# Kernel optimization log

Hardware: AMD Instinct MI355X
Metric: run time of the kernel (lower is better)

## Reference

```python
import jax, jax.numpy as jnp
import numpy as np
from jax import lax


def conv1x1(x, w, b=None):
    # x: [B,C,H,W], w: [O,C]
    y = jnp.einsum('bchw,oc->bohw', x, w)
    if b is not None:
        y = y + b[None, :, None, None]
    return y


def conv1x9(x, w, b):
    # x: [B,C,H,W], w: [O,I,1,9], pad (0,4) -> same spatial size
    y = lax.conv_general_dilated(x, w, window_strides=(1, 1),
                                 padding=((0, 0), (4, 4)),
                                 dimension_numbers=('NCHW', 'OIHW', 'NCHW'))
    return y + b[None, :, None, None]


def skn(inputs, fc1_w, fc2_w):
    # Selective Kernel fusion: M=len(inputs), each [B,C,H,W]
    M = len(inputs)
    B, C = inputs[0].shape[0], inputs[0].shape[1]
    U = inputs[0]
    for t in inputs[1:]:
        U = U + t
    s = U.mean(axis=(2, 3))                               # [B,C] global avg pool
    z = jax.nn.leaky_relu(jnp.einsum('bc,oc->bo', s, fc1_w), 0.01)
    ab = jnp.einsum('bo,po->bp', z, fc2_w).reshape(B, M, C)
    a = jax.nn.softmax(ab, axis=1)                        # softmax over branches
    out = inputs[0] * a[:, 0][:, :, None, None]
    for i in range(1, M):
        out = out + inputs[i] * a[:, i][:, :, None, None]
    return out


def setup_inputs() -> dict:
    key = jax.random.key(0)
    ks = jax.random.split(key, 24)
    B, C, H, W = 2, 128, 128, 512
    Ch = C // 2
    p = lambda k, shp: (jax.random.normal(k, shp, jnp.float32) * 0.02)
    d = {}
    d['left_feat'] = jax.random.normal(ks[0], (B, C, H, W), jnp.float32)
    d['right_feat'] = jax.random.normal(ks[1], (B, C, H, W), jnp.float32)
    d['emb_l_w'] = p(ks[2], (Ch, C)); d['emb_l_b'] = p(ks[3], (Ch,))
    d['emb_r_w'] = p(ks[4], (Ch, C)); d['emb_r_b'] = p(ks[5], (Ch,))
    d['emb_lv_w'] = p(ks[6], (Ch, C)); d['emb_lv_b'] = p(ks[7], (Ch,))
    d['emb_rv_w'] = p(ks[8], (Ch, C)); d['emb_rv_b'] = p(ks[9], (Ch,))
    d['out_l_w'] = p(ks[10], (C, Ch)); d['out_l_b'] = p(ks[11], (C,))
    d['head_w'] = p(ks[12], (C, 2 * C)); d['head_b'] = p(ks[13], (C,))
    d['body_w1'] = p(ks[14], (3, C, C, 1, 9)); d['body_b1'] = p(ks[15], (3, C))
    d['body_w2'] = p(ks[16], (3, C, C, 1, 9)); d['body_b2'] = p(ks[17], (3, C))
    d['skn1_fc1_w'] = p(ks[18], (C // 4, C)); d['skn1_fc2_w'] = p(ks[19], (3 * C, C // 4))
    d['skn2_fc1_w'] = p(ks[20], (C // 4, C)); d['skn2_fc2_w'] = p(ks[21], (3 * C, C // 4))
    d['num_window'] = 4
    return d


def reference(left_feat, right_feat, emb_l_w, emb_l_b, emb_r_w, emb_r_b,
              emb_lv_w, emb_lv_b, emb_rv_w, emb_rv_b, out_l_w, out_l_b,
              head_w, head_b, body_w1, body_b1, body_w2, body_b2,
              skn1_fc1_w, skn1_fc2_w, skn2_fc1_w, skn2_fc2_w, num_window):
    B, C, H, W = left_feat.shape
    Ch = C // 2
    nw = int(num_window)
    win = W // nw

    Q = conv1x1(left_feat, emb_l_w, emb_l_b)     # [B,Ch,H,W]
    K = conv1x1(right_feat, emb_r_w, emb_r_b)
    V_left = conv1x1(left_feat, emb_lv_w, emb_lv_b)   # computed but unused (source bug)
    V_right = conv1x1(right_feat, emb_rv_w, emb_rv_b)

    # windowed per-row cross attention over width
    Qw = Q.transpose(0, 2, 3, 1).reshape(B, H, nw, win, Ch)   # [B,H,n,q,c]
    Kw = K.transpose(0, 2, 3, 1).reshape(B, H, nw, win, Ch)   # [B,H,n,k,c]
    Vr = V_right.transpose(0, 2, 3, 1).reshape(B, H, nw, win, Ch)

    score = jnp.einsum('bhnqc,bhnkc->bhnqk', Qw, Kw)          # [B,H,n,q,k]
    M_r2l = jax.nn.softmax(score, axis=-1)
    out = jnp.einsum('bhnqk,bhnkc->bhnqc', M_r2l, Vr)         # [B,H,n,q,c]
    warped = out.reshape(B, H, W, Ch).transpose(0, 3, 1, 2)   # [B,Ch,H,W]
    left_feat_warped = jax.nn.relu(conv1x1(warped, out_l_w, out_l_b))
    # NOTE: source code (num_window>1 branch) reuses M_right_to_left and V_right
    # for the right warp as well -> right_feat_warped == left_feat_warped.
    right_feat_warped = left_feat_warped

    # head conv + 3 residual blocks (1x9 convs)
    mixed = jax.nn.relu(conv1x1(jnp.concatenate([left_feat, right_feat], axis=1),
                                head_w, head_b))
    x = mixed
    for i in range(3):
        r = jax.nn.relu(conv1x9(x, body_w1[i], body_b1[i]))
        r = conv1x9(r, body_w2[i], body_b2[i])
        x = x + r
    mixed_feat = x

    left_out = skn([left_feat, left_feat_warped, mixed_feat], skn1_fc1_w, skn1_fc2_w)
    right_out = skn([right_feat, right_feat_warped, mixed_feat], skn2_fc1_w, skn2_fc2_w)
    return (left_out, right_out)
```

## Files before the change

### kernel.cpp

```cpp
#include <hip/hip_runtime.h>
#include <hip/hip_bf16.h>

typedef __attribute__((ext_vector_type(8))) short bf16x8;
typedef __attribute__((ext_vector_type(4))) float f32x4;
typedef unsigned short u16;
typedef unsigned int u32;

#define DI __device__ __forceinline__
#define MFMA16(a, b, c) __builtin_amdgcn_mfma_f32_16x16x32_bf16((a), (b), (c), 0, 0, 0)

constexpr int Hh = 128, Ww = 512;
constexpr int HW = 65536;
constexpr long FULL = 16777216;
constexpr long HALF = 8388608;

__device__ __align__(16) u16 g_buf[2 * FULL];
__device__ __align__(16) u16 g_w[950272];
__device__ __align__(16) float g_bias[1216];
__device__ __align__(16) float g_fc[32768];
__device__ __align__(16) float g_pools[1024];
__device__ __align__(16) float g_gates[1536];
__device__ __align__(16) float g_ppart[524288];
__device__ int g_flag;

constexpr int EMB_L = 0, EMB_R = 8192, EMB_RV = 16384, HEAD = 24576, OUTL = 57344, BODY = 65536;
constexpr int B_EMBL = 0, B_EMBR = 64, B_EMBRV = 128, B_OUTL = 192, B_HEAD = 320, B_B1 = 448, B_B2 = 832;
constexpr int FC1A = 0, FC2A = 4096, FC1B = 16384, FC2B = 20480;

DI float b2f(u16 u) { union { u32 i; float f; } v; v.i = (u32)u << 16; return v.f; }
DI u16 f2b(float f) {
  union { float fl; u32 u; } v; v.fl = f;
  return (u16)((v.u + 0x7FFFu + ((v.u >> 16) & 1u)) >> 16);
}
DI float ldf(const void* p, long i, int f) {
  return f ? ((const float*)p)[i] : b2f(((const u16*)p)[i]);
}
DI bf16x8 ld8(const void* p) { return *reinterpret_cast<const bf16x8*>(p); }
DI void gload16(const u16* src, char* lds_dst) {
  __builtin_amdgcn_global_load_lds(
      (const __attribute__((address_space(1))) void*)src,
      (__attribute__((address_space(3))) void*)lds_dst, 16, 0, 0);
}

__global__ void k_detect(const void* left) {
  if (threadIdx.x != 0 || blockIdx.x != 0) return;
  const u16* pu = (const u16*)left;
  int okb = 0;
  for (int i = 0; i < 256; i++) {
    float x = b2f(pu[i]);
    float a = fabsf(x);
    if (x == 0.f || (a > 1e-8f && a < 1e4f)) okb++;
  }
  g_flag = (okb >= 230) ? 0 : 1;
}

__global__ void k_pack(const void* w1, const void* w2, const void* embl, const void* embr,
                       const void* embrv, const void* outl, const void* head,
                       const void* embl_b, const void* embr_b, const void* embrv_b,
                       const void* outl_b, const void* head_b, const void* b1, const void* b2,
                       const void* f1a, const void* f2a, const void* f1b, const void* f2b_) {
  int f = g_flag;
  int i = blockIdx.x * 256 + threadIdx.x;
  int job = blockIdx.y;
  if (job == 0) {
    if (i >= 884736) return;
    int c = i & 127, o = (i >> 7) & 127;
    int rest = i >> 14;
    int t = rest % 9, bc = rest / 9;
    const void* src = (bc & 1) ? w2 : w1;
    int blk = bc >> 1;
    g_w[BODY + i] = f2b(ldf(src, (((long)(blk * 128 + o) * 128 + c)) * 9 + t, f));
  } else if (job == 1) {
    if (i >= 65536) return;
    float v;
    if (i < 8192) v = ldf(embl, i, f);
    else if (i < 16384) v = ldf(embr, i - 8192, f);
    else if (i < 24576) v = ldf(embrv, i - 16384, f);
    else if (i < 57344) v = ldf(head, i - 24576, f);
    else v = ldf(outl, i - 57344, f);
    g_w[i] = f2b(v);
  } else if (job == 2) {
    if (i >= 1216) return;
    float v;
    if (i < 64) v = ldf(embl_b, i, f);
    else if (i < 128) v = ldf(embr_b, i - 64, f);
    else if (i < 192) v = ldf(embrv_b, i - 128, f);
    else if (i < 320) v = ldf(outl_b, i - 192, f);
    else if (i < 448) v = ldf(head_b, i - 320, f);
    else if (i < 832) v = ldf(b1, i - 448, f);
    else v = ldf(b2, i - 832, f);
    g_bias[i] = v;
  } else {
    if (i >= 32768) return;
    float v;
    if (i < 4096) v = ldf(f1a, i, f);
    else if (i < 16384) v = ldf(f2a, i - 4096, f);
    else if (i < 20480) v = ldf(f1b, i - 16384, f);
    else v = ldf(f2b_, i - 20480, f);
    g_fc[i] = v;
  }
}

__global__ __launch_bounds__(256) void k_nchw2nhwc(const void* srcL, const void* srcR,
                                                   u16* __restrict__ dstL, u16* __restrict__ dstR) {
  __shared__ u16 tile[64][130];
  int f = g_flag;
  int w0 = blockIdx.x * 64;
  int h = blockIdx.y;
  int b = blockIdx.z & 1;
  int img = blockIdx.z >> 1;
  const void* src = img ? srcR : srcL;
  u16* dst = img ? dstR : dstL;
  int t = threadIdx.x;
  int wq = (t & 31) * 2, cb = t >> 5;
  for (int c0 = 0; c0 < 128; c0 += 8) {
    int c = c0 + cb;
    long base = (long)(b * 128 + c) * HW + h * Ww + w0 + wq;
    if (f) {
      float2 v = *reinterpret_cast<const float2*>((const float*)src + base);
      tile[wq][c] = f2b(v.x);
      tile[wq + 1][c] = f2b(v.y);
    } else {
      u32 v = *reinterpret_cast<const u32*>((const u16*)src + base);
      tile[wq][c] = (u16)v;
      tile[wq + 1][c] = (u16)(v >> 16);
    }
  }
  __syncthreads();
  int c = t & 127, wb = t >> 7;
  long obase = (long)b * HW + (long)h * Ww + w0;
  for (int w1i = 0; w1i < 64; w1i += 2) {
    int w = w1i + wb;
    dst[(obase + w) * 128 + c] = tile[w][c];
  }
  if (t < 128) {
    float s = 0.f;
#pragma unroll
    for (int w = 0; w < 64; w++) s += b2f(tile[w][t]);
    g_ppart[((img * 2 + b) * 128 + t) * 1024 + (h * 8 + blockIdx.x)] = s;
  }
}

template<int K, int N, bool RELU, bool NCHW_OUT>
__global__ __launch_bounds__(256) void k_gemm1x1(const u16* __restrict__ xt, const u16* __restrict__ w,
                                                 const float* __restrict__ bias, u16* __restrict__ out,
                                                 int wstride) {
  extern __shared__ __align__(16) char smem[];
  constexpr int SLOTS = (K * 2) / 16;
  constexpr int RB = K * 2;
  int t = threadIdx.x;
  long p0 = (long)blockIdx.x * 128;
  for (int u = t; u < 128 * SLOTS; u += 256) {
    int row = u / SLOTS, slot = u % SLOTS;
    int4 v = *reinterpret_cast<const int4*>(xt + (p0 + row) * K + slot * 8);
    *reinterpret_cast<int4*>(smem + (((u32)(row * RB + slot * 16)) ^ ((row & 7) << 4))) = v;
  }
  __syncthreads();
  int wid = t >> 6, lane = t & 63, l15 = lane & 15, l4 = lane >> 4;
  constexpr int WAVES_M = (N == 64) ? 4 : 2;
  constexpr int MF = (128 / WAVES_M) / 16;
  int wm = (N == 64) ? wid : (wid >> 1);
  int wn = (N == 64) ? 0 : (wid & 1);
  int prow0 = wm * (128 / WAVES_M);
  int ocol0 = wn * 64;
  f32x4 zz = {0.f, 0.f, 0.f, 0.f};
  f32x4 acc[MF][4];
#pragma unroll
  for (int m = 0; m < MF; m++)
#pragma unroll
    for (int n = 0; n < 4; n++) acc[m][n] = zz;
#pragma unroll
  for (int k0 = 0; k0 < K; k0 += 32) {
    bf16x8 a[MF], bw[4];
#pragma unroll
    for (int m = 0; m < MF; m++) {
      int row = prow0 + m * 16 + l15;
      a[m] = ld8(smem + (((u32)(row * RB + (k0 + l4 * 8) * 2)) ^ ((row & 7) << 4)));
    }
#pragma unroll
    for (int n = 0; n < 4; n++) {
      int o = ocol0 + n * 16 + l15;
      bw[n] = ld8(w + (long)o * wstride + k0 + l4 * 8);
    }
#pragma unroll
    for (int m = 0; m < MF; m++)
#pragma unroll
      for (int n = 0; n < 4; n++) acc[m][n] = MFMA16(a[m], bw[n], acc[m][n]);
  }
  if constexpr (!NCHW_OUT) {
#pragma unroll
    for (int m = 0; m < MF; m++)
#pragma unroll
      for (int n = 0; n < 4; n++) {
        int o = ocol0 + n * 16 + l15;
        float bb = bias[o];
#pragma unroll
        for (int r = 0; r < 4; r++) {
          long p = p0 + prow0 + m * 16 + l4 * 4 + r;
          float v = acc[m][n][r] + bb;
          if (RELU) v = fmaxf(v, 0.f);
          out[p * N + o] = f2b(v);
        }
      }
  } else {
    __syncthreads();
    u16* tb = reinterpret_cast<u16*>(smem) + wid * (64 * 66);
#pragma unroll
    for (int m = 0; m < MF; m++)
#pragma unroll
      for (int n = 0; n < 4; n++) {
        float bb = bias[ocol0 + n * 16 + l15];
#pragma unroll
        for (int r = 0; r < 4; r++) {
          int pl = m * 16 + l4 * 4 + r;
          float v = acc[m][n][r] + bb;
          if (RELU) v = fmaxf(v, 0.f);
          tb[(n * 16 + l15) * 66 + pl] = f2b(v);
        }
      }
    __syncthreads();
    int bq = (int)(p0 / HW);
    int rem = (int)(p0 % HW);
    int hq = rem / Ww, wq0 = rem % Ww;
    for (int o = 0; o < 64; o++) {
      out[((long)(bq * 128 + ocol0 + o)) * HW + hq * Ww + wq0 + prow0 + lane] = tb[o * 66 + lane];
    }
  }
}

__global__ __launch_bounds__(256) void k_head(const u16* lt, const u16* rt,
                                              const u16* __restrict__ wh, const float* __restrict__ bh,
                                              u16* out) {
  extern __shared__ __align__(16) char smem[];
  int t = threadIdx.x;
  long p0 = (long)blockIdx.x * 128;
  for (int u = t; u < 2048; u += 256) {
    int row = u >> 4, slot = u & 15;
    u32 db = ((u32)(row * 256 + slot * 16)) ^ ((row & 7) << 4);
    *reinterpret_cast<int4*>(smem + db) = *reinterpret_cast<const int4*>(lt + (p0 + row) * 128 + slot * 8);
    *reinterpret_cast<int4*>(smem + 32768 + db) = *reinterpret_cast<const int4*>(rt + (p0 + row) * 128 + slot * 8);
  }
  __syncthreads();
  int wid = t >> 6, lane = t & 63, l15 = lane & 15, l4 = lane >> 4;
  int prow0 = (wid >> 1) * 64, ocol0 = (wid & 1) * 64;
  f32x4 zz = {0.f, 0.f, 0.f, 0.f};
  f32x4 acc[4][4];
#pragma unroll
  for (int m = 0; m < 4; m++)
#pragma unroll
    for (int n = 0; n < 4; n++) acc[m][n] = zz;
#pragma unroll
  for (int kk = 0; kk < 8; kk++) {
    int k0 = kk * 32;
    const char* sb = smem + ((kk >= 4) ? 32768 : 0);
    int kl = k0 & 127;
    bf16x8 a[4], bw[4];
#pragma unroll
    for (int m = 0; m < 4; m++) {
      int row = prow0 + m * 16 + l15;
      a[m] = ld8(sb + (((u32)(row * 256 + (kl + l4 * 8) * 2)) ^ ((row & 7) << 4)));
    }
#pragma unroll
    for (int n = 0; n < 4; n++) {
      int o = ocol0 + n * 16 + l15;
      bw[n] = ld8(wh + o * 256 + k0 + l4 * 8);
    }
#pragma unroll
    for (int m = 0; m < 4; m++)
#pragma unroll
      for (int n = 0; n < 4; n++) acc[m][n] = MFMA16(a[m], bw[n], acc[m][n]);
  }
  __syncthreads();
#pragma unroll
  for (int m = 0; m < 4; m++)
#pragma unroll
    for (int n = 0; n < 4; n++) {
      int o = ocol0 + n * 16 + l15;
      float bb = bh[o];
#pragma unroll
      for (int r = 0; r < 4; r++) {
        long p = p0 + prow0 + m * 16 + l4 * 4 + r;
        float v = fmaxf(acc[m][n][r] + bb, 0.f);
        out[p * 128 + o] = f2b(v);
      }
    }
}

__global__ __launch_bounds__(256) void k_attn(const u16* __restrict__ qt, const u16* __restrict__ kt,
                                              const u16* __restrict__ vt, u16* __restrict__ outT) {
  extern __shared__ __align__(16) char smem[];
  int n = blockIdx.x, h = blockIdx.y, b = blockIdx.z;
  long rb = ((long)(b * Hh + h)) * Ww + n * 128;
  int t = threadIdx.x;
  for (int u = t; u < 1024; u += 256) {
    int row = u >> 3, slot = u & 7;
    u32 db = ((u32)(row * 128 + slot * 16)) ^ ((row & 7) << 4);
    *reinterpret_cast<int4*>(smem + db) = *reinterpret_cast<const int4*>(qt + (rb + row) * 64 + slot * 8);
    *reinterpret_cast<int4*>(smem + 16384 + db) = *reinterpret_cast<const int4*>(kt + (rb + row) * 64 + slot * 8);
  }
  __syncthreads();
  int wid = t >> 6, lane = t & 63, l15 = lane & 15, l4 = lane >> 4;
  int q0 = wid * 32;
  f32x4 zz = {0.f, 0.f, 0.f, 0.f};
  f32x4 sc[2][8];
#pragma unroll
  for (int m = 0; m < 2; m++)
#pragma unroll
    for (int nf = 0; nf < 8; nf++) sc[m][nf] = zz;
#pragma unroll
  for (int k0 = 0; k0 < 64; k0 += 32) {
    bf16x8 aq[2], bk[8];
#pragma unroll
    for (int m = 0; m < 2; m++) {
      int row = q0 + m * 16 + l15;
      aq[m] = ld8(smem + (((u32)(row * 128 + (k0 + l4 * 8) * 2)) ^ ((row & 7) << 4)));
    }
#pragma unroll
    for (int nf = 0; nf < 8; nf++) {
      int row = nf * 16 + l15;
      bk[nf] = ld8(smem + 16384 + (((u32)(row * 128 + (k0 + l4 * 8) * 2)) ^ ((row & 7) << 4)));
    }
#pragma unroll
    for (int m = 0; m < 2; m++)
#pragma unroll
      for (int nf = 0; nf < 8; nf++) sc[m][nf] = MFMA16(aq[m], bk[nf], sc[m][nf]);
  }
  float rsum[2][4];
#pragma unroll
  for (int m = 0; m < 2; m++) {
#pragma unroll
    for (int r = 0; r < 4; r++) {
      float mx = -3.0e38f;
#pragma unroll
      for (int nf = 0; nf < 8; nf++) mx = fmaxf(mx, sc[m][nf][r]);
      mx = fmaxf(mx, __shfl_xor(mx, 1));
      mx = fmaxf(mx, __shfl_xor(mx, 2));
      mx = fmaxf(mx, __shfl_xor(mx, 4));
      mx = fmaxf(mx, __shfl_xor(mx, 8));
      int ql = q0 + m * 16 + l4 * 4 + r;
      float ssum = 0.f;
#pragma unroll
      for (int nf = 0; nf < 8; nf++) {
        float e = __expf(sc[m][nf][r] - mx);
        ssum += e;
        int k = nf * 16 + l15;
        *reinterpret_cast<u16*>(smem + 32768 + (((u32)(ql * 256 + k * 2)) ^ ((ql & 7) << 4))) = f2b(e);
      }
      ssum += __shfl_xor(ssum, 1);
      ssum += __shfl_xor(ssum, 2);
      ssum += __shfl_xor(ssum, 4);
      ssum += __shfl_xor(ssum, 8);
      rsum[m][r] = ssum;
    }
  }
  __syncthreads();
  for (int u = t; u < 8192; u += 256) {
    int k = u >> 6, c = u & 63;
    u16 v = vt[(rb + k) * 64 + c];
    *reinterpret_cast<u16*>(smem + (((u32)(c * 256 + k * 2)) ^ ((c & 7) << 4))) = v;
  }
  __syncthreads();
  f32x4 ov[2][4];
#pragma unroll
  for (int m = 0; m < 2; m++)
#pragma unroll
    for (int nf = 0; nf < 4; nf++) ov[m][nf] = zz;
#pragma unroll
  for (int k0 = 0; k0 < 128; k0 += 32) {
    bf16x8 ap[2], bv[4];
#pragma unroll
    for (int m = 0; m < 2; m++) {
      int row = q0 + m * 16 + l15;
      ap[m] = ld8(smem + 32768 + (((u32)(row * 256 + (k0 + l4 * 8) * 2)) ^ ((row & 7) << 4)));
    }
#pragma unroll
    for (int nf = 0; nf < 4; nf++) {
      int c = nf * 16 + l15;
      bv[nf] = ld8(smem + (((u32)(c * 256 + (k0 + l4 * 8) * 2)) ^ ((c & 7) << 4)));
    }
#pragma unroll
    for (int m = 0; m < 2; m++)
#pragma unroll
      for (int nf = 0; nf < 4; nf++) ov[m][nf] = MFMA16(ap[m], bv[nf], ov[m][nf]);
  }
#pragma unroll
  for (int m = 0; m < 2; m++)
#pragma unroll
    for (int nf = 0; nf < 4; nf++)
#pragma unroll
      for (int r = 0; r < 4; r++) {
        int q = q0 + m * 16 + l4 * 4 + r;
        int c = nf * 16 + l15;
        outT[(rb + q) * 64 + c] = f2b(ov[m][nf][r] / rsum[m][r]);
      }
}

template<bool RELU, bool HASRES, bool NCHW_OUT>
__global__ __launch_bounds__(256) void k_conv1x9(const u16* __restrict__ xin, const u16* __restrict__ wp9,
                                                 const float* __restrict__ bias, const u16* __restrict__ res,
                                                 u16* __restrict__ out) {
  __shared__ __align__(16) char xs[34816];
  __shared__ __align__(16) char wbuf[16384];
  int w0 = blockIdx.x * 128;
  int h = blockIdx.y, b = blockIdx.z;
  long rowg = ((long)(b * Hh + h)) * Ww;
  int t = threadIdx.x;
  int wid = t >> 6;
  auto stage = [&](int s) {
    int tap = s >> 2, kk = s & 3;
    const u16* base = wp9 + tap * 16384 + kk * 32;
#pragma unroll
    for (int j = 0; j < 2; j++) {
      int fidx = j * 256 + t;
      const u16* src = base + (fidx >> 2) * 128 + (fidx & 3) * 8;
      gload16(src, wbuf + (s & 1) * 8192 + j * 4096 + wid * 1024);
    }
  };
  for (int u = t; u < 2176; u += 256) {
    int row = u >> 4, slot = u & 15;
    int wg = w0 - 4 + row;
    int4 v{0, 0, 0, 0};
    if (wg >= 0 && wg < Ww) v = *reinterpret_cast<const int4*>(xin + (rowg + wg) * 128 + slot * 8);
    *reinterpret_cast<int4*>(xs + (((u32)(row * 256 + slot * 16)) ^ ((row & 7) << 4))) = v;
  }
  stage(0);
  __syncthreads();
  int lane = t & 63, l15 = lane & 15, l4 = lane >> 4;
  int p0w = (wid >> 1) * 64, o0w = (wid & 1) * 64;
  f32x4 zz = {0.f, 0.f, 0.f, 0.f};
  f32x4 acc[4][4];
#pragma unroll
  for (int m = 0; m < 4; m++)
#pragma unroll
    for (int n = 0; n < 4; n++) acc[m][n] = zz;
#pragma unroll 2
  for (int s = 0; s < 36; s++) {
    if (s < 35) stage(s + 1);
    int tap = s >> 2, kk = s & 3;
    bf16x8 a[4], bw[4];
#pragma unroll
    for (int n = 0; n < 4; n++)
      bw[n] = ld8(wbuf + (s & 1) * 8192 + (o0w + n * 16 + l15) * 64 + l4 * 16);
#pragma unroll
    for (int m = 0; m < 4; m++) {
      int row = p0w + m * 16 + l15 + tap;
      a[m] = ld8(xs + (((u32)(row * 256 + (kk * 32 + l4 * 8) * 2)) ^ ((row & 7) << 4)));
    }
#pragma unroll
    for (int m = 0; m < 4; m++)
#pragma unroll
      for (int n = 0; n < 4; n++) acc[m][n] = MFMA16(a[m], bw[n], acc[m][n]);
    __syncthreads();
  }
  float bb[4];
#pragma unroll
  for (int n = 0; n < 4; n++) bb[n] = bias[o0w + n * 16 + l15];
  if constexpr (!NCHW_OUT) {
#pragma unroll
    for (int m = 0; m < 4; m++)
#pragma unroll
      for (int n = 0; n < 4; n++) {
        int o = o0w + n * 16 + l15;
#pragma unroll
        for (int r = 0; r < 4; r++) {
          int p = w0 + p0w + m * 16 + l4 * 4 + r;
          float v = acc[m][n][r] + bb[n];
          if (RELU) v = fmaxf(v, 0.f);
          if (HASRES) v += b2f(res[(rowg + p) * 128 + o]);
          out[(rowg + p) * 128 + o] = f2b(v);
        }
      }
  } else {
    u16* tb = reinterpret_cast<u16*>(xs) + wid * (64 * 66);
#pragma unroll
    for (int m = 0; m < 4; m++)
#pragma unroll
      for (int n = 0; n < 4; n++) {
        int o = o0w + n * 16 + l15;
#pragma unroll
        for (int r = 0; r < 4; r++) {
          int pl = m * 16 + l4 * 4 + r;
          int p = w0 + p0w + pl;
          float v = acc[m][n][r] + bb[n];
          if (RELU) v = fmaxf(v, 0.f);
          if (HASRES) v += b2f(res[(rowg + p) * 128 + o]);
          tb[(n * 16 + l15) * 66 + pl] = f2b(v);
        }
      }
    __syncthreads();
    for (int o = 0; o < 64; o++) {
      out[((long)(b * 128 + o0w + o)) * HW + h * Ww + w0 + p0w + lane] = tb[o * 66 + lane];
    }
  }
}

__global__ __launch_bounds__(256) void k_pool(const u16* __restrict__ lfw, const u16* __restrict__ mixed) {
  int c = blockIdx.x, b = blockIdx.y, ts = blockIdx.z;
  float s = 0.f;
  if (ts < 2) {
    const float* pp = g_ppart + ((ts * 2 + b) * 128 + c) * 1024;
    for (int i = threadIdx.x; i < 1024; i += 256) s += pp[i];
  } else {
    long base = ((long)(b * 128 + c)) * HW;
    const u16* pu = (ts == 2) ? lfw + base : mixed + base;
    for (int i = threadIdx.x * 8; i < HW; i += 2048) {
      union { int4 v; u16 u[8]; } x;
      x.v = *reinterpret_cast<const int4*>(pu + i);
#pragma unroll
      for (int j = 0; j < 8; j++) s += b2f(x.u[j]);
    }
  }
#pragma unroll
  for (int m = 1; m < 64; m <<= 1) s += __shfl_xor(s, m);
  __shared__ float red[4];
  if ((threadIdx.x & 63) == 0) red[threadIdx.x >> 6] = s;
  __syncthreads();
  if (threadIdx.x == 0)
    g_pools[(ts * 2 + b) * 128 + c] = (red[0] + red[1] + red[2] + red[3]) * (1.f / HW);
}

__global__ void k_gate() {
  __shared__ float sv[128], zv[32];
  int b = blockIdx.x, s = blockIdx.y;
  int t = threadIdx.x;
  sv[t] = g_pools[(s * 2 + b) * 128 + t] + g_pools[(4 + b) * 128 + t] + g_pools[(6 + b) * 128 + t];
  __syncthreads();
  const float* fc1 = g_fc + (s ? FC1B : FC1A);
  const float* fc2 = g_fc + (s ? FC2B : FC2A);
  if (t < 32) {
    float z = 0.f;
    for (int c = 0; c < 128; c++) z += fc1[t * 128 + c] * sv[c];
    zv[t] = (z > 0.f) ? z : 0.01f * z;
  }
  __syncthreads();
  float ab[3];
#pragma unroll
  for (int i = 0; i < 3; i++) {
    float a = 0.f;
    for (int j = 0; j < 32; j++) a += fc2[(i * 128 + t) * 32 + j] * zv[j];
    ab[i] = a;
  }
  float mx = fmaxf(ab[0], fmaxf(ab[1], ab[2]));
  float e0 = __expf(ab[0] - mx), e1 = __expf(ab[1] - mx), e2 = __expf(ab[2] - mx);
  float inv = 1.f / (e0 + e1 + e2);
  g_gates[((s * 2 + b) * 3 + 0) * 128 + t] = e0 * inv;
  g_gates[((s * 2 + b) * 3 + 1) * 128 + t] = e1 * inv;
  g_gates[((s * 2 + b) * 3 + 2) * 128 + t] = e2 * inv;
}

__global__ __launch_bounds__(256) void k_skn_out(const void* left, const void* right,
                                                 const u16* __restrict__ lfw, const u16* __restrict__ mixed,
                                                 void* doutv) {
  int chunk = blockIdx.x, c = blockIdx.y, b = blockIdx.z;
  int f = g_flag;
  const float* g1 = g_gates + (b * 3) * 128 + c;
  const float* g2 = g_gates + ((2 + b) * 3) * 128 + c;
  float a10 = g1[0], a11 = g1[128], a12 = g1[256];
  float a20 = g2[0], a21 = g2[128], a22 = g2[256];
  long off = ((long)(b * 128 + c)) * HW + chunk * 2048 + threadIdx.x * 8;
  float xl[8], xr[8];
  if (f) {
    const float* L = (const float*)left + off;
    const float* R = (const float*)right + off;
    float4 a0 = *reinterpret_cast<const float4*>(L);
    float4 a1 = *reinterpret_cast<const float4*>(L + 4);
    float4 r0 = *reinterpret_cast<const float4*>(R);
    float4 r1 = *reinterpret_cast<const float4*>(R + 4);
    xl[0]=a0.x; xl[1]=a0.y; xl[2]=a0.z; xl[3]=a0.w; xl[4]=a1.x; xl[5]=a1.y; xl[6]=a1.z; xl[7]=a1.w;
    xr[0]=r0.x; xr[1]=r0.y; xr[2]=r0.z; xr[3]=r0.w; xr[4]=r1.x; xr[5]=r1.y; xr[6]=r1.z; xr[7]=r1.w;
  } else {
    union { int4 v; u16 u[8]; } a, r;
    a.v = *reinterpret_cast<const int4*>((const u16*)left + off);
    r.v = *reinterpret_cast<const int4*>((const u16*)right + off);
#pragma unroll
    for (int j = 0; j < 8; j++) { xl[j] = b2f(a.u[j]); xr[j] = b2f(r.u[j]); }
  }
  union { int4 v; u16 u[8]; } vw, vm;
  vw.v = *reinterpret_cast<const int4*>(lfw + off);
  vm.v = *reinterpret_cast<const int4*>(mixed + off);
  float ol[8], orr[8];
#pragma unroll
  for (int j = 0; j < 8; j++) {
    float fw = b2f(vw.u[j]), fm = b2f(vm.u[j]);
    ol[j] = a10 * xl[j] + a11 * fw + a12 * fm;
    orr[j] = a20 * xr[j] + a21 * fw + a22 * fm;
  }
  if (f) {
    float* fo = (float*)doutv;
    *reinterpret_cast<float4*>(fo + off) = make_float4(ol[0], ol[1], ol[2], ol[3]);
    *reinterpret_cast<float4*>(fo + off + 4) = make_float4(ol[4], ol[5], ol[6], ol[7]);
    *reinterpret_cast<float4*>(fo + FULL + off) = make_float4(orr[0], orr[1], orr[2], orr[3]);
    *reinterpret_cast<float4*>(fo + FULL + off + 4) = make_float4(orr[4], orr[5], orr[6], orr[7]);
  } else {
    u16* bo = (u16*)doutv;
    union { int4 v; u16 u[8]; } o1, o2;
#pragma unroll
    for (int j = 0; j < 8; j++) { o1.u[j] = f2b(ol[j]); o2.u[j] = f2b(orr[j]); }
    *reinterpret_cast<int4*>(bo + off) = o1.v;
    *reinterpret_cast<int4*>(bo + FULL + off) = o2.v;
  }
}

extern "C" void kernel_launch(void* const* d_in, const int* in_sizes, int n_in,
                              void* d_out, int out_size, void* d_ws, size_t ws_size,
                              hipStream_t stream) {
  (void)in_sizes; (void)n_in; (void)out_size; (void)d_ws; (void)ws_size;
  const void* left    = d_in[0];
  const void* right   = d_in[1];

  u16* gbuf = nullptr;
  (void)hipGetSymbolAddress((void**)&gbuf, HIP_SYMBOL(g_buf));
  u16* gw = nullptr;
  (void)hipGetSymbolAddress((void**)&gw, HIP_SYMBOL(g_w));
  float* gbias = nullptr;
  (void)hipGetSymbolAddress((void**)&gbias, HIP_SYMBOL(g_bias));

  u16* du = (u16*)d_out;
  u16* leftT   = du;
  u16* rA      = du;
  u16* rightT  = du + FULL;
  u16* xG      = du + FULL;
  u16* QT      = gbuf;
  u16* KT      = gbuf + HALF;
  u16* VrT     = gbuf + FULL;
  u16* warpedT = gbuf + FULL + HALF;
  u16* lfw     = gbuf;
  u16* mixed   = gbuf + FULL;

  k_detect<<<dim3(1), dim3(64), 0, stream>>>(left);
  k_pack<<<dim3(3456, 4), dim3(256), 0, stream>>>(
      d_in[14], d_in[16], d_in[2], d_in[4], d_in[8], d_in[10], d_in[12],
      d_in[3], d_in[5], d_in[9], d_in[11], d_in[13], d_in[15], d_in[17],
      d_in[18], d_in[19], d_in[20], d_in[21]);
  k_nchw2nhwc<<<dim3(8, 128, 4), dim3(256), 0, stream>>>(left, right, leftT, rightT);
  k_gemm1x1<128, 64, false, false><<<dim3(1024), dim3(256), 32768, stream>>>(leftT, gw + EMB_L, gbias + B_EMBL, QT, 128);
  k_gemm1x1<128, 64, false, false><<<dim3(1024), dim3(256), 32768, stream>>>(rightT, gw + EMB_R, gbias + B_EMBR, KT, 128);
  k_gemm1x1<128, 64, false, false><<<dim3(1024), dim3(256), 32768, stream>>>(rightT, gw + EMB_RV, gbias + B_EMBRV, VrT, 128);
  k_head<<<dim3(1024), dim3(256), 65536, stream>>>(leftT, rightT, gw + HEAD, gbias + B_HEAD, xG);
  k_attn<<<dim3(4, 128, 2), dim3(256), 65536, stream>>>(QT, KT, VrT, warpedT);
  k_gemm1x1<64, 128, true, true><<<dim3(1024), dim3(256), 33792, stream>>>(warpedT, gw + OUTL, gbias + B_OUTL, lfw, 64);
  for (int i = 0; i < 3; i++) {
    k_conv1x9<true, false, false><<<dim3(4, 128, 2), dim3(256), 0, stream>>>(
        xG, gw + BODY + (long)(i * 2 + 0) * 9 * 16384, gbias + B_B1 + i * 128, nullptr, rA);
    if (i < 2)
      k_conv1x9<false, true, false><<<dim3(4, 128, 2), dim3(256), 0, stream>>>(
          rA, gw + BODY + (long)(i * 2 + 1) * 9 * 16384, gbias + B_B2 + i * 128, xG, xG);
    else
      k_conv1x9<false, true, true><<<dim3(4, 128, 2), dim3(256), 0, stream>>>(
          rA, gw + BODY + (long)(i * 2 + 1) * 9 * 16384, gbias + B_B2 + i * 128, xG, mixed);
  }
  k_pool<<<dim3(128, 2, 4), dim3(256), 0, stream>>>(lfw, mixed);
  k_gate<<<dim3(2, 2), dim3(128), 0, stream>>>();
  k_skn_out<<<dim3(32, 128, 2), dim3(256), 0, stream>>>(left, right, lfw, mixed, d_out);
}
```

Baseline: 581.9 us.

## Triple-buffer conv1x9 weight staging with prefetch distance two and swizzled LDS

The 1x9 conv kernel moves from a double-buffered weight stage to a three-slot ring that prefetches two K-steps ahead. Each iteration now waits with explicit vmcnt counts and a raw s_barrier instead of a full __syncthreads, so global-to-LDS weight loads can overlap more MFMA work. Weight rows are also XOR-swizzled in LDS to reduce bank conflicts on the B-fragment reads. In exchange it uses more LDS per block, which may lower occupancy, and the correctness of the hand-written waitcnt counts depends on how gload16 is lowered.

```diff
diff --git a/kernel.cpp b/kernel.cpp
--- a/kernel.cpp
+++ b/kernel.cpp
@@ -400,20 +400,21 @@
                                                  const float* __restrict__ bias, const u16* __restrict__ res,
                                                  u16* __restrict__ out) {
   __shared__ __align__(16) char xs[34816];
-  __shared__ __align__(16) char wbuf[16384];
+  __shared__ __align__(16) char wbuf[24576];
   int w0 = blockIdx.x * 128;
   int h = blockIdx.y, b = blockIdx.z;
   long rowg = ((long)(b * Hh + h)) * Ww;
   int t = threadIdx.x;
   int wid = t >> 6;
-  auto stage = [&](int s) {
+  auto stage = [&](int s, int buf) {
     int tap = s >> 2, kk = s & 3;
     const u16* base = wp9 + tap * 16384 + kk * 32;
 #pragma unroll
     for (int j = 0; j < 2; j++) {
-      int fidx = j * 256 + t;
-      const u16* src = base + (fidx >> 2) * 128 + (fidx & 3) * 8;
-      gload16(src, wbuf + (s & 1) * 8192 + j * 4096 + wid * 1024);
+      int u = j * 256 + t;
+      int o = u >> 2, sl = u & 3;
+      int l = sl ^ (o & 3);
+      gload16(base + o * 128 + l * 8, wbuf + buf * 8192 + j * 4096 + wid * 1024);
     }
   };
   for (int u = t; u < 2176; u += 256) {
@@ -423,8 +424,11 @@
     if (wg >= 0 && wg < Ww) v = *reinterpret_cast<const int4*>(xin + (rowg + wg) * 128 + slot * 8);
     *reinterpret_cast<int4*>(xs + (((u32)(row * 256 + slot * 16)) ^ ((row & 7) << 4))) = v;
   }
-  stage(0);
-  __syncthreads();
+  stage(0, 0);
+  stage(1, 1);
+  asm volatile("s_waitcnt vmcnt(2) lgkmcnt(0)" ::: "memory");
+  __builtin_amdgcn_s_barrier();
+  __builtin_amdgcn_sched_barrier(0);
   int lane = t & 63, l15 = lane & 15, l4 = lane >> 4;
   int p0w = (wid >> 1) * 64, o0w = (wid & 1) * 64;
   f32x4 zz = {0.f, 0.f, 0.f, 0.f};
@@ -433,24 +437,35 @@
   for (int m = 0; m < 4; m++)
 #pragma unroll
     for (int n = 0; n < 4; n++) acc[m][n] = zz;
-#pragma unroll 2
+  int bcur = 0;
+#pragma unroll 1
   for (int s = 0; s < 36; s++) {
-    if (s < 35) stage(s + 1);
+    if (s < 34) {
+      int b2i = bcur + 2; if (b2i >= 3) b2i -= 3;
+      stage(s + 2, b2i);
+    }
     int tap = s >> 2, kk = s & 3;
+    const char* wb = wbuf + bcur * 8192;
     bf16x8 a[4], bw[4];
 #pragma unroll
-    for (int n = 0; n < 4; n++)
-      bw[n] = ld8(wbuf + (s & 1) * 8192 + (o0w + n * 16 + l15) * 64 + l4 * 16);
+    for (int n = 0; n < 4; n++) {
+      int o = o0w + n * 16 + l15;
+      bw[n] = ld8(wb + o * 64 + ((l4 ^ (o & 3)) * 16));
+    }
 #pragma unroll
     for (int m = 0; m < 4; m++) {
       int row = p0w + m * 16 + l15 + tap;
-      a[m] = ld8(xs + (((u32)(row * 256 + (kk * 32 + l4 * 8) * 2)) ^ ((row & 7) << 4)));
+      a[m] = ld8(xs + (((u32)(row * 256 + kk * 64 + l4 * 16)) ^ ((row & 7) << 4)));
     }
 #pragma unroll
     for (int m = 0; m < 4; m++)
 #pragma unroll
       for (int n = 0; n < 4; n++) acc[m][n] = MFMA16(a[m], bw[n], acc[m][n]);
-    __syncthreads();
+    if (s < 34) asm volatile("s_waitcnt vmcnt(2)" ::: "memory");
+    else        asm volatile("s_waitcnt vmcnt(0)" ::: "memory");
+    __builtin_amdgcn_s_barrier();
+    __builtin_amdgcn_sched_barrier(0);
+    bcur = bcur + 1; if (bcur >= 3) bcur -= 3;
   }
   float bb[4];
 #pragma unroll
```

After: 638.0 us. +9.6%, slower.

## Merge embedding GEMMs into one launch and drop per-step barriers in conv1x9

Applied to the files above, without the earlier changes.

The three 1x1 embedding GEMMs become one kernel launched on a 3-row grid, with weights read straight from global memory. In conv1x9, each wave now stages its own 64-output weight slice into a private double buffer with a rotated layout. This lets the per-iteration __syncthreads be replaced by a vmcnt wait, and MFMA priority is raised around the compute. The goal is to remove block-wide barrier stalls across the six conv launches and two launch overheads. The cost is larger LDS per block and per-wave duplicated weight loads, and correctness relies on the hand-written vmcnt accounting.

```diff
diff --git a/kernel.cpp b/kernel.cpp
--- a/kernel.cpp
+++ b/kernel.cpp
@@ -228,6 +228,63 @@
   }
 }
 
+__global__ __launch_bounds__(256) void k_emb3(const u16* __restrict__ leftT, const u16* __restrict__ rightT,
+                                              const u16* __restrict__ gw, const float* __restrict__ gbias,
+                                              u16* __restrict__ QT, u16* __restrict__ KT, u16* __restrict__ VrT) {
+  extern __shared__ __align__(16) char smem[];
+  int br = blockIdx.y;
+  const u16* xt = (br == 0) ? leftT : rightT;
+  const u16* w = gw + ((br == 0) ? EMB_L : (br == 1) ? EMB_R : EMB_RV);
+  const float* bias = gbias + ((br == 0) ? B_EMBL : (br == 1) ? B_EMBR : B_EMBRV);
+  u16* out = (br == 0) ? QT : (br == 1) ? KT : VrT;
+  int t = threadIdx.x;
+  long p0 = (long)blockIdx.x * 128;
+  for (int u = t; u < 2048; u += 256) {
+    int row = u >> 4, slot = u & 15;
+    int4 v = *reinterpret_cast<const int4*>(xt + (p0 + row) * 128 + slot * 8);
+    *reinterpret_cast<int4*>(smem + (((u32)(row * 256 + slot * 16)) ^ ((row & 7) << 4))) = v;
+  }
+  __syncthreads();
+  int wid = t >> 6, lane = t & 63, l15 = lane & 15, l4 = lane >> 4;
+  int prow0 = wid * 32;
+  f32x4 zz = {0.f, 0.f, 0.f, 0.f};
+  f32x4 acc[2][4];
+#pragma unroll
+  for (int m = 0; m < 2; m++)
+#pragma unroll
+    for (int n = 0; n < 4; n++) acc[m][n] = zz;
+#pragma unroll
+  for (int k0 = 0; k0 < 128; k0 += 32) {
+    bf16x8 a[2], bw[4];
+#pragma unroll
+    for (int m = 0; m < 2; m++) {
+      int row = prow0 + m * 16 + l15;
+      a[m] = ld8(smem + (((u32)(row * 256 + (k0 + l4 * 8) * 2)) ^ ((row & 7) << 4)));
+    }
+#pragma unroll
+    for (int n = 0; n < 4; n++) {
+      int o = n * 16 + l15;
+      bw[n] = ld8(w + (long)o * 128 + k0 + l4 * 8);
+    }
+#pragma unroll
+    for (int m = 0; m < 2; m++)
+#pragma unroll
+      for (int n = 0; n < 4; n++) acc[m][n] = MFMA16(a[m], bw[n], acc[m][n]);
+  }
+#pragma unroll
+  for (int m = 0; m < 2; m++)
+#pragma unroll
+    for (int n = 0; n < 4; n++) {
+      int o = n * 16 + l15;
+      float bb = bias[o];
+#pragma unroll
+      for (int r = 0; r < 4; r++) {
+        long p = p0 + prow0 + m * 16 + l4 * 4 + r;
+        out[p * 64 + o] = f2b(acc[m][n][r] + bb);
+      }
+    }
+}
+
 __global__ __launch_bounds__(256) void k_head(const u16* lt, const u16* rt,
                                               const u16* __restrict__ wh, const float* __restrict__ bh,
                                               u16* out) {
@@ -400,20 +457,23 @@
                                                  const float* __restrict__ bias, const u16* __restrict__ res,
                                                  u16* __restrict__ out) {
   __shared__ __align__(16) char xs[34816];
-  __shared__ __align__(16) char wbuf[16384];
+  __shared__ __align__(16) char wbuf[32768];
   int w0 = blockIdx.x * 128;
   int h = blockIdx.y, b = blockIdx.z;
   long rowg = ((long)(b * Hh + h)) * Ww;
   int t = threadIdx.x;
-  int wid = t >> 6;
+  int wid = t >> 6, lane = t & 63;
+  int o0w = (wid & 1) * 64;
+  char* wbase = wbuf + wid * 8192;
   auto stage = [&](int s) {
     int tap = s >> 2, kk = s & 3;
-    const u16* base = wp9 + tap * 16384 + kk * 32;
-#pragma unroll
-    for (int j = 0; j < 2; j++) {
-      int fidx = j * 256 + t;
-      const u16* src = base + (fidx >> 2) * 128 + (fidx & 3) * 8;
-      gload16(src, wbuf + (s & 1) * 8192 + j * 4096 + wid * 1024);
+    const u16* base = wp9 + tap * 16384 + (long)o0w * 128 + kk * 32;
+#pragma unroll
+    for (int j = 0; j < 4; j++) {
+      int u = j * 64 + lane;
+      int op = u >> 2, p = u & 3;
+      int l = (p - (op >> 1)) & 3;
+      gload16(base + op * 128 + l * 8, wbase + (s & 1) * 4096 + j * 1024);
     }
   };
   for (int u = t; u < 2176; u += 256) {
@@ -425,32 +485,42 @@
   }
   stage(0);
   __syncthreads();
-  int lane = t & 63, l15 = lane & 15, l4 = lane >> 4;
-  int p0w = (wid >> 1) * 64, o0w = (wid & 1) * 64;
+  int l15 = lane & 15, l4 = lane >> 4;
+  int p0w = (wid >> 1) * 64;
   f32x4 zz = {0.f, 0.f, 0.f, 0.f};
   f32x4 acc[4][4];
 #pragma unroll
   for (int m = 0; m < 4; m++)
 #pragma unroll
     for (int n = 0; n < 4; n++) acc[m][n] = zz;
-#pragma unroll 2
+#pragma unroll 1
   for (int s = 0; s < 36; s++) {
-    if (s < 35) stage(s + 1);
+    if (s < 35) {
+      stage(s + 1);
+      asm volatile("s_waitcnt vmcnt(4)" ::: "memory");
+    } else {
+      asm volatile("s_waitcnt vmcnt(0)" ::: "memory");
+    }
     int tap = s >> 2, kk = s & 3;
+    const char* wb = wbase + (s & 1) * 4096;
     bf16x8 a[4], bw[4];
 #pragma unroll
-    for (int n = 0; n < 4; n++)
-      bw[n] = ld8(wbuf + (s & 1) * 8192 + (o0w + n * 16 + l15) * 64 + l4 * 16);
+    for (int n = 0; n < 4; n++) {
+      int op = n * 16 + l15;
+      int p = (l4 + (op >> 1)) & 3;
+      bw[n] = ld8(wb + op * 64 + p * 16);
+    }
 #pragma unroll
     for (int m = 0; m < 4; m++) {
       int row = p0w + m * 16 + l15 + tap;
-      a[m] = ld8(xs + (((u32)(row * 256 + (kk * 32 + l4 * 8) * 2)) ^ ((row & 7) << 4)));
-    }
+      a[m] = ld8(xs + (((u32)(row * 256 + kk * 64 + l4 * 16)) ^ ((row & 7) << 4)));
+    }
+    __builtin_amdgcn_s_setprio(1);
 #pragma unroll
     for (int m = 0; m < 4; m++)
 #pragma unroll
       for (int n = 0; n < 4; n++) acc[m][n] = MFMA16(a[m], bw[n], acc[m][n]);
-    __syncthreads();
+    __builtin_amdgcn_s_setprio(0);
   }
   float bb[4];
 #pragma unroll
@@ -471,6 +541,7 @@
         }
       }
   } else {
+    __syncthreads();
     u16* tb = reinterpret_cast<u16*>(xs) + wid * (64 * 66);
 #pragma unroll
     for (int m = 0; m < 4; m++)
@@ -633,9 +704,7 @@
       d_in[3], d_in[5], d_in[9], d_in[11], d_in[13], d_in[15], d_in[17],
       d_in[18], d_in[19], d_in[20], d_in[21]);
   k_nchw2nhwc<<<dim3(8, 128, 4), dim3(256), 0, stream>>>(left, right, leftT, rightT);
-  k_gemm1x1<128, 64, false, false><<<dim3(1024), dim3(256), 32768, stream>>>(leftT, gw + EMB_L, gbias + B_EMBL, QT, 128);
-  k_gemm1x1<128, 64, false, false><<<dim3(1024), dim3(256), 32768, stream>>>(rightT, gw + EMB_R, gbias + B_EMBR, KT, 128);
-  k_gemm1x1<128, 64, false, false><<<dim3(1024), dim3(256), 32768, stream>>>(rightT, gw + EMB_RV, gbias + B_EMBRV, VrT, 128);
+  k_emb3<<<dim3(1024, 3), dim3(256), 32768, stream>>>(leftT, rightT, gw, gbias, QT, KT, VrT);
   k_head<<<dim3(1024), dim3(256), 65536, stream>>>(leftT, rightT, gw + HEAD, gbias + B_HEAD, xG);
   k_attn<<<dim3(4, 128, 2), dim3(256), 65536, stream>>>(QT, KT, VrT, warpedT);
   k_gemm1x1<64, 128, true, true><<<dim3(1024), dim3(256), 33792, stream>>>(warpedT, gw + OUTL, gbias + B_OUTL, lfw, 64);
```

Result: no change. 590.8 us (+1.5%).
